# Kernel tuning notes

Hardware: AMD Instinct MI355X
Metric: run time of the kernel (lower is better)

The kernel has to match this reference:

```python
import jax, jax.numpy as jnp
import numpy as np

N_NODES = 100000
N_EDGES = 1600000
D_IN = 128
D_OUT = 128


def setup_inputs() -> dict:
    key = jax.random.key(0)
    k1, k2, k3 = jax.random.split(key, 3)
    x = jax.random.normal(k1, (N_NODES, D_IN), dtype=jnp.float32)
    edge_index = jax.random.randint(k2, (2, N_EDGES), 0, N_NODES, dtype=jnp.int32)
    W = jax.random.normal(k3, (D_IN, D_OUT), dtype=jnp.float32) / np.sqrt(D_IN)
    b = jnp.zeros((D_OUT,), dtype=jnp.float32)
    return {"x": x, "edge_index": edge_index, "W": W, "b": b}


def reference(x, edge_index, W, b):
    """GCNConv (add self-loops, symmetric norm) + ReLU.
    out = relu(D^-1/2 (A+I) D^-1/2 X W + b)
    """
    N = x.shape[0]
    src, dst = edge_index[0], edge_index[1]
    loop = jnp.arange(N, dtype=src.dtype)
    src = jnp.concatenate([src, loop])  # [E+N]
    dst = jnp.concatenate([dst, loop])  # [E+N]

    # degree of target nodes (includes self-loop, so deg >= 1)
    deg = jax.ops.segment_sum(jnp.ones(dst.shape, dtype=x.dtype), dst,
                              num_segments=N)
    deg_inv_sqrt = jax.lax.rsqrt(deg)
    norm = deg_inv_sqrt[src] * deg_inv_sqrt[dst]  # [E+N]

    h = x @ W  # [N, D_OUT] — transform before aggregation (PyG GCNConv)
    msg = h[src] * norm[:, None]  # gather + normalize
    out = jax.ops.segment_sum(msg, dst, num_segments=N)  # scatter-add
    return jax.nn.relu(out + b)
```

## Files before the change

### kernel.cpp

```cpp
#include <hip/hip_runtime.h>

#define N_NODES 100000
#define N_EDGES 1600000
#define D 128
#define SUBW 32
#define NSUB2 3125
#define NC 196
#define BSH 9
#define BMSK 511
#define CAPC 12288
#define CAP3 9728
#define CAPS2 1024
#define CHUNK3 4096
#define BIND_BLOCKS ((N_EDGES + CHUNK3 - 1) / CHUNK3)
#define GEMM_BLOCKS ((N_NODES + 63) / 64)
#define STAGE_MAX (CHUNK3 + NC * 16)
#define NGRP (STAGE_MAX / 16)
#define CCSTRIDE 16

typedef __attribute__((ext_vector_type(8))) short short8;
typedef __attribute__((ext_vector_type(4))) float float4v;

__device__ inline unsigned short f2bf(float f) {
    unsigned u = __float_as_uint(f);
    unsigned r = (u + 0x7fffu + ((u >> 16) & 1u)) >> 16;
    return (unsigned short)r;
}
__device__ inline float bflo(unsigned int p) { return __uint_as_float(p << 16); }
__device__ inline float bfhi(unsigned int p) { return __uint_as_float(p & 0xffff0000u); }

__global__ void probe_convert_kernel(const unsigned int* __restrict__ xw,
                                     const void* __restrict__ b,
                                     int* __restrict__ flag, float* __restrict__ bfv,
                                     int* __restrict__ ccnt) {
    __shared__ int cnt;
    if (threadIdx.x == 0) cnt = 0;
    __syncthreads();
    unsigned low = xw[threadIdx.x] & 0xFFFFu;
    unsigned e = (low >> 7) & 0xFFu;
    atomicAdd(&cnt, (int)((e == 0u) || (e >= 107u && e <= 147u)));
    __syncthreads();
    int m = (cnt >= 192);
    if (threadIdx.x == 0) *flag = m;
    if (threadIdx.x < D)
        bfv[threadIdx.x] = m ? bflo(((const unsigned short*)b)[threadIdx.x])
                             : ((const float*)b)[threadIdx.x];
    for (int i = threadIdx.x; i < NC * CCSTRIDE; i += 256) ccnt[i] = 0;
}

__global__ void __launch_bounds__(256) fused_bingemm_kernel(
        const int* __restrict__ src, const int* __restrict__ dst,
        int* __restrict__ ccnt, unsigned* __restrict__ recg,
        const void* __restrict__ xv, const void* __restrict__ Wv,
        const int* __restrict__ flag, unsigned short* __restrict__ h) {
    __shared__ union {
        struct {
            unsigned stg[STAGE_MAX];
            int cnt[NC], cpad[NC], ofs[NC], base[NC], place[NC];
            unsigned short g2b[NGRP];
            int tot;
        } b;
        unsigned short Wt[D * 136];
    } u;

    int tid = threadIdx.x;

    if (blockIdx.x < BIND_BLOCKS) {
        int e0 = blockIdx.x * CHUNK3;
        int e1 = e0 + CHUNK3 < N_EDGES ? e0 + CHUNK3 : N_EDGES;
        if (tid < NC) u.b.cnt[tid] = 0;
        __syncthreads();

        unsigned recs[16];
        int bks[16];
        #pragma unroll
        for (int k = 0; k < 4; ++k) {
            int i = e0 + tid * 4 + k * 1024;
            if (i + 3 < e1) {
                int4 d4 = *(const int4*)&dst[i];
                int4 s4 = *(const int4*)&src[i];
                recs[k * 4 + 0] = (unsigned)s4.x | ((unsigned)(d4.x & BMSK) << 17); bks[k * 4 + 0] = d4.x >> BSH;
                recs[k * 4 + 1] = (unsigned)s4.y | ((unsigned)(d4.y & BMSK) << 17); bks[k * 4 + 1] = d4.y >> BSH;
                recs[k * 4 + 2] = (unsigned)s4.z | ((unsigned)(d4.z & BMSK) << 17); bks[k * 4 + 2] = d4.z >> BSH;
                recs[k * 4 + 3] = (unsigned)s4.w | ((unsigned)(d4.w & BMSK) << 17); bks[k * 4 + 3] = d4.w >> BSH;
            } else {
                bks[k * 4 + 0] = -1; bks[k * 4 + 1] = -1; bks[k * 4 + 2] = -1; bks[k * 4 + 3] = -1;
                recs[k * 4 + 0] = 0; recs[k * 4 + 1] = 0; recs[k * 4 + 2] = 0; recs[k * 4 + 3] = 0;
            }
        }
        #pragma unroll
        for (int k = 0; k < 16; ++k)
            if (bks[k] >= 0) atomicAdd(&u.b.cnt[bks[k]], 1);
        __syncthreads();

        if (tid < NC) {
            int c = u.b.cnt[tid];
            int p = (c + 15) & ~15;
            u.b.cpad[tid] = p;
            u.b.base[tid] = p ? atomicAdd(&ccnt[tid * CCSTRIDE], p) : 0;
        }
        __syncthreads();
        if (tid == 0) {
            int s = 0;
            for (int k = 0; k < NC; ++k) { u.b.ofs[k] = s; u.b.place[k] = s; s += u.b.cpad[k]; }
            u.b.tot = s;
        }
        __syncthreads();
        if (tid < NC) {
            int o = u.b.ofs[tid], e = o + u.b.cpad[tid];
            for (int j = o + u.b.cnt[tid]; j < e; ++j) u.b.stg[j] = 0xFFFFFFFFu;
            for (int g = o >> 4; g < (e >> 4); ++g) u.b.g2b[g] = (unsigned short)tid;
        }
        __syncthreads();

        #pragma unroll
        for (int k = 0; k < 16; ++k)
            if (bks[k] >= 0) {
                int p = atomicAdd(&u.b.place[bks[k]], 1);
                u.b.stg[p] = recs[k];
            }
        __syncthreads();

        int tot_ = u.b.tot;
        for (int j = tid * 4; j < tot_; j += 1024) {
            int lo = u.b.g2b[j >> 4];
            int gi = u.b.base[lo] + (j - u.b.ofs[lo]);
            if (gi < CAPC)
                *(uint4*)&recg[(size_t)lo * CAPC + gi] = *(const uint4*)&u.b.stg[j];
        }
    } else {
        int bid2 = blockIdx.x - BIND_BLOCKS;
        int m = *flag;
        for (int idx = tid; idx < D * D; idx += 256) {
            int k = idx >> 7, c = idx & 127;
            u.Wt[c * 136 + k] = m ? ((const unsigned short*)Wv)[idx]
                                  : f2bf(((const float*)Wv)[idx]);
        }
        __syncthreads();

        int wave = tid >> 6, lane = tid & 63;
        int row0 = (bid2 * 4 + wave) * 16;
        if (row0 >= N_NODES) return;
        int r = lane & 15, quad = lane >> 4;

        short8 a[4];
        if (m) {
            const unsigned short* xr = (const unsigned short*)xv + (size_t)(row0 + r) * D + quad * 8;
            #pragma unroll
            for (int t = 0; t < 4; ++t) a[t] = *(const short8*)(xr + t * 32);
        } else {
            const float* xr = (const float*)xv + (size_t)(row0 + r) * D + quad * 8;
            #pragma unroll
            for (int t = 0; t < 4; ++t) {
                float4 f0 = *(const float4*)(xr + t * 32);
                float4 f1 = *(const float4*)(xr + t * 32 + 4);
                a[t][0] = (short)f2bf(f0.x); a[t][1] = (short)f2bf(f0.y);
                a[t][2] = (short)f2bf(f0.z); a[t][3] = (short)f2bf(f0.w);
                a[t][4] = (short)f2bf(f1.x); a[t][5] = (short)f2bf(f1.y);
                a[t][6] = (short)f2bf(f1.z); a[t][7] = (short)f2bf(f1.w);
            }
        }

        #pragma unroll
        for (int ct = 0; ct < 8; ++ct) {
            int col0 = ct * 16;
            float4v c = {0.f, 0.f, 0.f, 0.f};
            #pragma unroll
            for (int t = 0; t < 4; ++t) {
                short8 bfr = *(const short8*)&u.Wt[(col0 + r) * 136 + t * 32 + quad * 8];
                c = __builtin_amdgcn_mfma_f32_16x16x32_bf16(a[t], bfr, c, 0, 0, 0);
            }
            #pragma unroll
            for (int reg = 0; reg < 4; ++reg) {
                int orow = row0 + quad * 4 + reg;
                h[(size_t)orow * D + col0 + r] = f2bf(c[reg]);
            }
        }
    }
}

__global__ void __launch_bounds__(1024) sortdeg_kernel(
        unsigned* __restrict__ recg, const int* __restrict__ ccnt,
        int* __restrict__ deg, int* __restrict__ nodeofs, float* __restrict__ dis) {
    __shared__ int hist[512];
    __shared__ int ofs[512];
    __shared__ int place[512];
    __shared__ int wsum[8];
    __shared__ __align__(16) unsigned s_srt[CAP3];

    int b = blockIdx.x, tid = threadIdx.x;
    if (tid < 512) hist[tid] = 0;
    __syncthreads();
    int count = ccnt[b * CCSTRIDE]; if (count > CAPC) count = CAPC;
    const unsigned* r = recg + (size_t)b * CAPC;
    for (int i = tid * 4; i + 3 < count; i += 4096) {
        uint4 w4 = *(const uint4*)&r[i];
        if (w4.x != 0xFFFFFFFFu) atomicAdd(&hist[w4.x >> 17], 1);
        if (w4.y != 0xFFFFFFFFu) atomicAdd(&hist[w4.y >> 17], 1);
        if (w4.z != 0xFFFFFFFFu) atomicAdd(&hist[w4.z >> 17], 1);
        if (w4.w != 0xFFFFFFFFu) atomicAdd(&hist[w4.w >> 17], 1);
    }
    __syncthreads();

    int lane = tid & 63, wave = tid >> 6;
    int h0 = 0, v = 0;
    if (tid < 512) {
        h0 = hist[tid];
        v = h0;
        #pragma unroll
        for (int dsh = 1; dsh < 64; dsh <<= 1) {
            int uu = __shfl_up(v, dsh);
            if (lane >= dsh) v += uu;
        }
        if (lane == 63) wsum[wave] = v;
    }
    __syncthreads();
    if (tid < 512) {
        int wbase = 0;
        #pragma unroll
        for (int k = 0; k < 8; ++k) if (k < wave) wbase += wsum[k];
        int e0v = wbase + v - h0;
        ofs[tid] = e0v; place[tid] = e0v;
        int n = b * 512 + tid;
        deg[n] = h0;
        nodeofs[n] = e0v;
        dis[n] = rsqrtf((float)(h0 + 1));
    }
    __syncthreads();

    for (int i = tid * 4; i + 3 < count; i += 4096) {
        uint4 w4 = *(const uint4*)&r[i];
        if (w4.x != 0xFFFFFFFFu) { int p = atomicAdd(&place[w4.x >> 17], 1); if (p < CAP3) s_srt[p] = w4.x & 0x1FFFFu; }
        if (w4.y != 0xFFFFFFFFu) { int p = atomicAdd(&place[w4.y >> 17], 1); if (p < CAP3) s_srt[p] = w4.y & 0x1FFFFu; }
        if (w4.z != 0xFFFFFFFFu) { int p = atomicAdd(&place[w4.z >> 17], 1); if (p < CAP3) s_srt[p] = w4.z & 0x1FFFFu; }
        if (w4.w != 0xFFFFFFFFu) { int p = atomicAdd(&place[w4.w >> 17], 1); if (p < CAP3) s_srt[p] = w4.w & 0x1FFFFu; }
    }
    __syncthreads();

    int total = ofs[511] + hist[511];
    int totR = (total + 15) & ~15; if (totR > CAP3) totR = CAP3;
    unsigned* w = recg + (size_t)b * CAPC;
    for (int j = tid * 4; j < totR; j += 4096)
        *(uint4*)&w[j] = *(const uint4*)&s_srt[j];
}

__global__ void __launch_bounds__(256) agg5_kernel(
        const unsigned* __restrict__ srt2, const int* __restrict__ nodeofs,
        const int* __restrict__ deg, const float* __restrict__ dis,
        const float* __restrict__ bfv, const int* __restrict__ flag,
        const unsigned short* __restrict__ h, void* __restrict__ out) {
    __shared__ unsigned srt[CAPS2];
    __shared__ int l_ofs[SUBW];
    __shared__ int l_deg[SUBW];
    __shared__ float lbias[D];

    int sub = blockIdx.x, tid = threadIdx.x;
    int n0 = sub * SUBW;
    int B = n0 >> BSH, loc0 = n0 & BMSK;
    if (tid < SUBW) {
        l_ofs[tid] = nodeofs[B * 512 + loc0 + tid];
        l_deg[tid] = deg[n0 + tid];
    }
    if (tid < D) lbias[tid] = bfv[tid];
    __syncthreads();

    int base0 = l_ofs[0];
    int span = (l_ofs[SUBW - 1] + l_deg[SUBW - 1]) - base0;
    if (span > CAPS2) span = CAPS2;
    if (span > CAP3 - base0) span = CAP3 - base0;
    const unsigned* sb = srt2 + (size_t)B * CAPC + base0;
    for (int i = tid; i < span; i += 256) srt[i] = sb[i];
    __syncthreads();

    const uint4* h4 = (const uint4*)h;
    int wave = tid >> 6, lane = tid & 63;
    int q = lane >> 4, c16 = lane & 15;
    int m = *flag;

    for (int t = 0; t < 8; ++t) {
        int nl = wave * 8 + t;
        int n = n0 + nl;
        int o = l_ofs[nl] - base0;
        int cnt = l_deg[nl];
        int e_end = o + cnt; if (e_end > span) e_end = span;

        uint4 sp = make_uint4(0u, 0u, 0u, 0u);
        if (q == 0) sp = h4[(size_t)n * 16 + c16];

        float acc[8] = {0.f, 0.f, 0.f, 0.f, 0.f, 0.f, 0.f, 0.f};
        int j = o + q;
        for (; j + 4 < e_end; j += 8) {
            unsigned s0 = srt[j];
            unsigned s1 = srt[j + 4];
            uint4 p0 = h4[(size_t)s0 * 16 + c16];
            uint4 p1 = h4[(size_t)s1 * 16 + c16];
            float w0 = dis[s0], w1 = dis[s1];
            acc[0] += w0 * bflo(p0.x); acc[1] += w0 * bfhi(p0.x);
            acc[2] += w0 * bflo(p0.y); acc[3] += w0 * bfhi(p0.y);
            acc[4] += w0 * bflo(p0.z); acc[5] += w0 * bfhi(p0.z);
            acc[6] += w0 * bflo(p0.w); acc[7] += w0 * bfhi(p0.w);
            acc[0] += w1 * bflo(p1.x); acc[1] += w1 * bfhi(p1.x);
            acc[2] += w1 * bflo(p1.y); acc[3] += w1 * bfhi(p1.y);
            acc[4] += w1 * bflo(p1.z); acc[5] += w1 * bfhi(p1.z);
            acc[6] += w1 * bflo(p1.w); acc[7] += w1 * bfhi(p1.w);
        }
        if (j < e_end) {
            unsigned s0 = srt[j];
            uint4 p0 = h4[(size_t)s0 * 16 + c16];
            float w0 = dis[s0];
            acc[0] += w0 * bflo(p0.x); acc[1] += w0 * bfhi(p0.x);
            acc[2] += w0 * bflo(p0.y); acc[3] += w0 * bfhi(p0.y);
            acc[4] += w0 * bflo(p0.z); acc[5] += w0 * bfhi(p0.z);
            acc[6] += w0 * bflo(p0.w); acc[7] += w0 * bfhi(p0.w);
        }
        #pragma unroll
        for (int i = 0; i < 8; ++i) {
            acc[i] += __shfl_xor(acc[i], 16);
            acc[i] += __shfl_xor(acc[i], 32);
        }

        if (q == 0) {
            float dn = rsqrtf((float)(cnt + 1));
            float v[8];
            v[0] = fmaxf(dn * (acc[0] + dn * bflo(sp.x)) + lbias[c16 * 8 + 0], 0.f);
            v[1] = fmaxf(dn * (acc[1] + dn * bfhi(sp.x)) + lbias[c16 * 8 + 1], 0.f);
            v[2] = fmaxf(dn * (acc[2] + dn * bflo(sp.y)) + lbias[c16 * 8 + 2], 0.f);
            v[3] = fmaxf(dn * (acc[3] + dn * bfhi(sp.y)) + lbias[c16 * 8 + 3], 0.f);
            v[4] = fmaxf(dn * (acc[4] + dn * bflo(sp.z)) + lbias[c16 * 8 + 4], 0.f);
            v[5] = fmaxf(dn * (acc[5] + dn * bfhi(sp.z)) + lbias[c16 * 8 + 5], 0.f);
            v[6] = fmaxf(dn * (acc[6] + dn * bflo(sp.w)) + lbias[c16 * 8 + 6], 0.f);
            v[7] = fmaxf(dn * (acc[7] + dn * bfhi(sp.w)) + lbias[c16 * 8 + 7], 0.f);
            if (m) {
                uint4 pk;
                pk.x = ((unsigned)f2bf(v[1]) << 16) | f2bf(v[0]);
                pk.y = ((unsigned)f2bf(v[3]) << 16) | f2bf(v[2]);
                pk.z = ((unsigned)f2bf(v[5]) << 16) | f2bf(v[4]);
                pk.w = ((unsigned)f2bf(v[7]) << 16) | f2bf(v[6]);
                ((uint4*)out)[(size_t)n * 16 + c16] = pk;
            } else {
                float4 f0 = make_float4(v[0], v[1], v[2], v[3]);
                float4 f1 = make_float4(v[4], v[5], v[6], v[7]);
                float4* of = (float4*)((float*)out + (size_t)n * D + c16 * 8);
                of[0] = f0; of[1] = f1;
            }
        }
    }
}

extern "C" void kernel_launch(void* const* d_in, const int* in_sizes, int n_in,
                              void* d_out, int out_size, void* d_ws, size_t ws_size,
                              hipStream_t stream) {
    const void* x = nullptr; const int* ei = nullptr;
    const void* W = nullptr; const void* b = nullptr;
    for (int i = 0; i < n_in; ++i) {
        if      (in_sizes[i] == N_NODES * D) x  = d_in[i];
        else if (in_sizes[i] == 2 * N_EDGES) ei = (const int*)d_in[i];
        else if (in_sizes[i] == D * D)       W  = d_in[i];
        else if (in_sizes[i] == D)           b  = d_in[i];
    }
    if (!x || !ei || !W || !b) {
        x = d_in[0]; ei = (const int*)d_in[1]; W = d_in[2]; b = d_in[3];
    }
    const int* src = ei;
    const int* dst = ei + N_EDGES;

    char* ws = (char*)d_ws;
    int*      flag    = (int*)ws;
    int*      ccnt    = (int*)(ws + 16);
    float*    bfv     = (float*)(ccnt + NC * CCSTRIDE);
    int*      deg     = (int*)(bfv + D);
    int*      nodeofs = deg + NC * 512;
    float*    dis     = (float*)(nodeofs + NC * 512);
    unsigned* recg    = (unsigned*)(dis + NC * 512);
    unsigned short* h = (unsigned short*)(recg + (size_t)NC * CAPC);

    probe_convert_kernel<<<1, 256, 0, stream>>>((const unsigned int*)x, b, flag, bfv, ccnt);

    fused_bingemm_kernel<<<BIND_BLOCKS + GEMM_BLOCKS, 256, 0, stream>>>(
        src, dst, ccnt, recg, x, W, flag, h);

    sortdeg_kernel<<<NC, 1024, 0, stream>>>(recg, ccnt, deg, nodeofs, dis);

    agg5_kernel<<<NSUB2, 256, 0, stream>>>(recg, nodeofs, deg, dis, bfv, flag, h, d_out);
}
```

Measured before the change: 244.1 us.

## Refuse GEMM with per-bucket sort instead of binning; preconvert W once

```diff
diff --git a/kernel.cpp b/kernel.cpp
--- a/kernel.cpp
+++ b/kernel.cpp
@@ -13,7 +13,7 @@
 #define CAPS2 1024
 #define CHUNK3 4096
 #define BIND_BLOCKS ((N_EDGES + CHUNK3 - 1) / CHUNK3)
-#define GEMM_BLOCKS ((N_NODES + 63) / 64)
+#define GEMM2_BLOCKS ((N_NODES + 127) / 128)
 #define STAGE_MAX (CHUNK3 + NC * 16)
 #define NGRP (STAGE_MAX / 16)
 #define CCSTRIDE 16
@@ -31,7 +31,9 @@
 
 __global__ void probe_convert_kernel(const unsigned int* __restrict__ xw,
                                      const void* __restrict__ b,
+                                     const void* __restrict__ Wv,
                                      int* __restrict__ flag, float* __restrict__ bfv,
+                                     unsigned short* __restrict__ Wbf,
                                      int* __restrict__ ccnt) {
     __shared__ int cnt;
     if (threadIdx.x == 0) cnt = 0;
@@ -45,101 +47,160 @@
     if (threadIdx.x < D)
         bfv[threadIdx.x] = m ? bflo(((const unsigned short*)b)[threadIdx.x])
                              : ((const float*)b)[threadIdx.x];
+    for (int i = threadIdx.x; i < D * D; i += 256)
+        Wbf[i] = m ? ((const unsigned short*)Wv)[i] : f2bf(((const float*)Wv)[i]);
     for (int i = threadIdx.x; i < NC * CCSTRIDE; i += 256) ccnt[i] = 0;
 }
 
-__global__ void __launch_bounds__(256) fused_bingemm_kernel(
+__global__ void __launch_bounds__(256) binD_kernel(
         const int* __restrict__ src, const int* __restrict__ dst,
-        int* __restrict__ ccnt, unsigned* __restrict__ recg,
-        const void* __restrict__ xv, const void* __restrict__ Wv,
+        int* __restrict__ ccnt, unsigned* __restrict__ recg) {
+    __shared__ __align__(16) unsigned stg[STAGE_MAX];
+    __shared__ int cnt[NC], cpad[NC], ofs[NC], base[NC], place[NC];
+    __shared__ unsigned short g2b[NGRP];
+    __shared__ int tot;
+
+    int tid = threadIdx.x;
+    int e0 = blockIdx.x * CHUNK3;
+    int e1 = e0 + CHUNK3 < N_EDGES ? e0 + CHUNK3 : N_EDGES;
+    if (tid < NC) cnt[tid] = 0;
+    __syncthreads();
+
+    unsigned recs[16];
+    int bks[16];
+    #pragma unroll
+    for (int k = 0; k < 4; ++k) {
+        int i = e0 + tid * 4 + k * 1024;
+        if (i + 3 < e1) {
+            int4 d4 = *(const int4*)&dst[i];
+            int4 s4 = *(const int4*)&src[i];
+            recs[k * 4 + 0] = (unsigned)s4.x | ((unsigned)(d4.x & BMSK) << 17); bks[k * 4 + 0] = d4.x >> BSH;
+            recs[k * 4 + 1] = (unsigned)s4.y | ((unsigned)(d4.y & BMSK) << 17); bks[k * 4 + 1] = d4.y >> BSH;
+            recs[k * 4 + 2] = (unsigned)s4.z | ((unsigned)(d4.z & BMSK) << 17); bks[k * 4 + 2] = d4.z >> BSH;
+            recs[k * 4 + 3] = (unsigned)s4.w | ((unsigned)(d4.w & BMSK) << 17); bks[k * 4 + 3] = d4.w >> BSH;
+        } else {
+            bks[k * 4 + 0] = -1; bks[k * 4 + 1] = -1; bks[k * 4 + 2] = -1; bks[k * 4 + 3] = -1;
+            recs[k * 4 + 0] = 0; recs[k * 4 + 1] = 0; recs[k * 4 + 2] = 0; recs[k * 4 + 3] = 0;
+        }
+    }
+    #pragma unroll
+    for (int k = 0; k < 16; ++k)
+        if (bks[k] >= 0) atomicAdd(&cnt[bks[k]], 1);
+    __syncthreads();
+
+    if (tid < NC) {
+        int c = cnt[tid];
+        int p = (c + 15) & ~15;
+        cpad[tid] = p;
+        base[tid] = p ? atomicAdd(&ccnt[tid * CCSTRIDE], p) : 0;
+    }
+    __syncthreads();
+    if (tid == 0) {
+        int s = 0;
+        for (int k = 0; k < NC; ++k) { ofs[k] = s; place[k] = s; s += cpad[k]; }
+        tot = s;
+    }
+    __syncthreads();
+    if (tid < NC) {
+        int o = ofs[tid], e = o + cpad[tid];
+        for (int j = o + cnt[tid]; j < e; ++j) stg[j] = 0xFFFFFFFFu;
+        for (int g = o >> 4; g < (e >> 4); ++g) g2b[g] = (unsigned short)tid;
+    }
+    __syncthreads();
+
+    #pragma unroll
+    for (int k = 0; k < 16; ++k)
+        if (bks[k] >= 0) {
+            int p = atomicAdd(&place[bks[k]], 1);
+            stg[p] = recs[k];
+        }
+    __syncthreads();
+
+    int tot_ = tot;
+    for (int j = tid * 4; j < tot_; j += 1024) {
+        int lo = g2b[j >> 4];
+        int gi = base[lo] + (j - ofs[lo]);
+        if (gi < CAPC)
+            *(uint4*)&recg[(size_t)lo * CAPC + gi] = *(const uint4*)&stg[j];
+    }
+}
+
+__global__ void __launch_bounds__(512) fused_sortgemm_kernel(
+        unsigned* __restrict__ recg, const int* __restrict__ ccnt,
+        int* __restrict__ deg, int* __restrict__ nodeofs, float* __restrict__ dis,
+        const void* __restrict__ xv, const unsigned short* __restrict__ Wbf,
         const int* __restrict__ flag, unsigned short* __restrict__ h) {
     __shared__ union {
         struct {
-            unsigned stg[STAGE_MAX];
-            int cnt[NC], cpad[NC], ofs[NC], base[NC], place[NC];
-            unsigned short g2b[NGRP];
-            int tot;
-        } b;
+            int hist[512], ofs[512], place[512], wsum[8];
+            __align__(16) unsigned s_srt[CAP3];
+        } s;
         unsigned short Wt[D * 136];
     } u;
 
     int tid = threadIdx.x;
 
-    if (blockIdx.x < BIND_BLOCKS) {
-        int e0 = blockIdx.x * CHUNK3;
-        int e1 = e0 + CHUNK3 < N_EDGES ? e0 + CHUNK3 : N_EDGES;
-        if (tid < NC) u.b.cnt[tid] = 0;
-        __syncthreads();
-
-        unsigned recs[16];
-        int bks[16];
+    if (blockIdx.x < NC) {
+        int b = blockIdx.x;
+        u.s.hist[tid] = 0;
+        __syncthreads();
+        int count = ccnt[b * CCSTRIDE]; if (count > CAPC) count = CAPC;
+        const unsigned* r = recg + (size_t)b * CAPC;
+        for (int i = tid * 4; i + 3 < count; i += 2048) {
+            uint4 w4 = *(const uint4*)&r[i];
+            if (w4.x != 0xFFFFFFFFu) atomicAdd(&u.s.hist[w4.x >> 17], 1);
+            if (w4.y != 0xFFFFFFFFu) atomicAdd(&u.s.hist[w4.y >> 17], 1);
+            if (w4.z != 0xFFFFFFFFu) atomicAdd(&u.s.hist[w4.z >> 17], 1);
+            if (w4.w != 0xFFFFFFFFu) atomicAdd(&u.s.hist[w4.w >> 17], 1);
+        }
+        __syncthreads();
+
+        int lane = tid & 63, wave = tid >> 6;
+        int h0 = u.s.hist[tid];
+        int v = h0;
         #pragma unroll
-        for (int k = 0; k < 4; ++k) {
-            int i = e0 + tid * 4 + k * 1024;
-            if (i + 3 < e1) {
-                int4 d4 = *(const int4*)&dst[i];
-                int4 s4 = *(const int4*)&src[i];
-                recs[k * 4 + 0] = (unsigned)s4.x | ((unsigned)(d4.x & BMSK) << 17); bks[k * 4 + 0] = d4.x >> BSH;
-                recs[k * 4 + 1] = (unsigned)s4.y | ((unsigned)(d4.y & BMSK) << 17); bks[k * 4 + 1] = d4.y >> BSH;
-                recs[k * 4 + 2] = (unsigned)s4.z | ((unsigned)(d4.z & BMSK) << 17); bks[k * 4 + 2] = d4.z >> BSH;
-                recs[k * 4 + 3] = (unsigned)s4.w | ((unsigned)(d4.w & BMSK) << 17); bks[k * 4 + 3] = d4.w >> BSH;
-            } else {
-                bks[k * 4 + 0] = -1; bks[k * 4 + 1] = -1; bks[k * 4 + 2] = -1; bks[k * 4 + 3] = -1;
-                recs[k * 4 + 0] = 0; recs[k * 4 + 1] = 0; recs[k * 4 + 2] = 0; recs[k * 4 + 3] = 0;
-            }
-        }
+        for (int dsh = 1; dsh < 64; dsh <<= 1) {
+            int uu = __shfl_up(v, dsh);
+            if (lane >= dsh) v += uu;
+        }
+        if (lane == 63) u.s.wsum[wave] = v;
+        __syncthreads();
+        int wbase = 0;
         #pragma unroll
-        for (int k = 0; k < 16; ++k)
-            if (bks[k] >= 0) atomicAdd(&u.b.cnt[bks[k]], 1);
-        __syncthreads();
-
-        if (tid < NC) {
-            int c = u.b.cnt[tid];
-            int p = (c + 15) & ~15;
-            u.b.cpad[tid] = p;
-            u.b.base[tid] = p ? atomicAdd(&ccnt[tid * CCSTRIDE], p) : 0;
-        }
-        __syncthreads();
-        if (tid == 0) {
-            int s = 0;
-            for (int k = 0; k < NC; ++k) { u.b.ofs[k] = s; u.b.place[k] = s; s += u.b.cpad[k]; }
-            u.b.tot = s;
-        }
-        __syncthreads();
-        if (tid < NC) {
-            int o = u.b.ofs[tid], e = o + u.b.cpad[tid];
-            for (int j = o + u.b.cnt[tid]; j < e; ++j) u.b.stg[j] = 0xFFFFFFFFu;
-            for (int g = o >> 4; g < (e >> 4); ++g) u.b.g2b[g] = (unsigned short)tid;
-        }
-        __syncthreads();
-
-        #pragma unroll
-        for (int k = 0; k < 16; ++k)
-            if (bks[k] >= 0) {
-                int p = atomicAdd(&u.b.place[bks[k]], 1);
-                u.b.stg[p] = recs[k];
-            }
-        __syncthreads();
-
-        int tot_ = u.b.tot;
-        for (int j = tid * 4; j < tot_; j += 1024) {
-            int lo = u.b.g2b[j >> 4];
-            int gi = u.b.base[lo] + (j - u.b.ofs[lo]);
-            if (gi < CAPC)
-                *(uint4*)&recg[(size_t)lo * CAPC + gi] = *(const uint4*)&u.b.stg[j];
-        }
+        for (int k = 0; k < 8; ++k) if (k < wave) wbase += u.s.wsum[k];
+        int e0v = wbase + v - h0;
+        u.s.ofs[tid] = e0v; u.s.place[tid] = e0v;
+        int n = b * 512 + tid;
+        deg[n] = h0;
+        nodeofs[n] = e0v;
+        dis[n] = rsqrtf((float)(h0 + 1));
+        __syncthreads();
+
+        for (int i = tid * 4; i + 3 < count; i += 2048) {
+            uint4 w4 = *(const uint4*)&r[i];
+            if (w4.x != 0xFFFFFFFFu) { int p = atomicAdd(&u.s.place[w4.x >> 17], 1); if (p < CAP3) u.s.s_srt[p] = w4.x & 0x1FFFFu; }
+            if (w4.y != 0xFFFFFFFFu) { int p = atomicAdd(&u.s.place[w4.y >> 17], 1); if (p < CAP3) u.s.s_srt[p] = w4.y & 0x1FFFFu; }
+            if (w4.z != 0xFFFFFFFFu) { int p = atomicAdd(&u.s.place[w4.z >> 17], 1); if (p < CAP3) u.s.s_srt[p] = w4.z & 0x1FFFFu; }
+            if (w4.w != 0xFFFFFFFFu) { int p = atomicAdd(&u.s.place[w4.w >> 17], 1); if (p < CAP3) u.s.s_srt[p] = w4.w & 0x1FFFFu; }
+        }
+        __syncthreads();
+
+        int total = u.s.ofs[511] + u.s.hist[511];
+        int totR = (total + 15) & ~15; if (totR > CAP3) totR = CAP3;
+        unsigned* w = recg + (size_t)b * CAPC;
+        for (int j = tid * 4; j < totR; j += 2048)
+            *(uint4*)&w[j] = *(const uint4*)&u.s.s_srt[j];
     } else {
-        int bid2 = blockIdx.x - BIND_BLOCKS;
+        int bid2 = blockIdx.x - NC;
         int m = *flag;
-        for (int idx = tid; idx < D * D; idx += 256) {
+        for (int idx = tid; idx < D * D; idx += 512) {
             int k = idx >> 7, c = idx & 127;
-            u.Wt[c * 136 + k] = m ? ((const unsigned short*)Wv)[idx]
-                                  : f2bf(((const float*)Wv)[idx]);
+            u.Wt[c * 136 + k] = Wbf[idx];
         }
         __syncthreads();
 
         int wave = tid >> 6, lane = tid & 63;
-        int row0 = (bid2 * 4 + wave) * 16;
+        int row0 = (bid2 * 8 + wave) * 16;
         if (row0 >= N_NODES) return;
         int r = lane & 15, quad = lane >> 4;
 
@@ -177,71 +238,6 @@
             }
         }
     }
-}
-
-__global__ void __launch_bounds__(1024) sortdeg_kernel(
-        unsigned* __restrict__ recg, const int* __restrict__ ccnt,
-        int* __restrict__ deg, int* __restrict__ nodeofs, float* __restrict__ dis) {
-    __shared__ int hist[512];
-    __shared__ int ofs[512];
-    __shared__ int place[512];
-    __shared__ int wsum[8];
-    __shared__ __align__(16) unsigned s_srt[CAP3];
-
-    int b = blockIdx.x, tid = threadIdx.x;
-    if (tid < 512) hist[tid] = 0;
-    __syncthreads();
-    int count = ccnt[b * CCSTRIDE]; if (count > CAPC) count = CAPC;
-    const unsigned* r = recg + (size_t)b * CAPC;
-    for (int i = tid * 4; i + 3 < count; i += 4096) {
-        uint4 w4 = *(const uint4*)&r[i];
-        if (w4.x != 0xFFFFFFFFu) atomicAdd(&hist[w4.x >> 17], 1);
-        if (w4.y != 0xFFFFFFFFu) atomicAdd(&hist[w4.y >> 17], 1);
-        if (w4.z != 0xFFFFFFFFu) atomicAdd(&hist[w4.z >> 17], 1);
-        if (w4.w != 0xFFFFFFFFu) atomicAdd(&hist[w4.w >> 17], 1);
-    }
-    __syncthreads();
-
-    int lane = tid & 63, wave = tid >> 6;
-    int h0 = 0, v = 0;
-    if (tid < 512) {
-        h0 = hist[tid];
-        v = h0;
-        #pragma unroll
-        for (int dsh = 1; dsh < 64; dsh <<= 1) {
-            int uu = __shfl_up(v, dsh);
-            if (lane >= dsh) v += uu;
-        }
-        if (lane == 63) wsum[wave] = v;
-    }
-    __syncthreads();
-    if (tid < 512) {
-        int wbase = 0;
-        #pragma unroll
-        for (int k = 0; k < 8; ++k) if (k < wave) wbase += wsum[k];
-        int e0v = wbase + v - h0;
-        ofs[tid] = e0v; place[tid] = e0v;
-        int n = b * 512 + tid;
-        deg[n] = h0;
-        nodeofs[n] = e0v;
-        dis[n] = rsqrtf((float)(h0 + 1));
-    }
-    __syncthreads();
-
-    for (int i = tid * 4; i + 3 < count; i += 4096) {
-        uint4 w4 = *(const uint4*)&r[i];
-        if (w4.x != 0xFFFFFFFFu) { int p = atomicAdd(&place[w4.x >> 17], 1); if (p < CAP3) s_srt[p] = w4.x & 0x1FFFFu; }
-        if (w4.y != 0xFFFFFFFFu) { int p = atomicAdd(&place[w4.y >> 17], 1); if (p < CAP3) s_srt[p] = w4.y & 0x1FFFFu; }
-        if (w4.z != 0xFFFFFFFFu) { int p = atomicAdd(&place[w4.z >> 17], 1); if (p < CAP3) s_srt[p] = w4.z & 0x1FFFFu; }
-        if (w4.w != 0xFFFFFFFFu) { int p = atomicAdd(&place[w4.w >> 17], 1); if (p < CAP3) s_srt[p] = w4.w & 0x1FFFFu; }
-    }
-    __syncthreads();
-
-    int total = ofs[511] + hist[511];
-    int totR = (total + 15) & ~15; if (totR > CAP3) totR = CAP3;
-    unsigned* w = recg + (size_t)b * CAPC;
-    for (int j = tid * 4; j < totR; j += 4096)
-        *(uint4*)&w[j] = *(const uint4*)&s_srt[j];
 }
 
 __global__ void __launch_bounds__(256) agg5_kernel(
@@ -368,18 +364,20 @@
     int*      flag    = (int*)ws;
     int*      ccnt    = (int*)(ws + 16);
     float*    bfv     = (float*)(ccnt + NC * CCSTRIDE);
-    int*      deg     = (int*)(bfv + D);
+    unsigned short* Wbf = (unsigned short*)(bfv + D);
+    int*      deg     = (int*)(Wbf + D * D);
     int*      nodeofs = deg + NC * 512;
     float*    dis     = (float*)(nodeofs + NC * 512);
     unsigned* recg    = (unsigned*)(dis + NC * 512);
     unsigned short* h = (unsigned short*)(recg + (size_t)NC * CAPC);
 
-    probe_convert_kernel<<<1, 256, 0, stream>>>((const unsigned int*)x, b, flag, bfv, ccnt);
-
-    fused_bingemm_kernel<<<BIND_BLOCKS + GEMM_BLOCKS, 256, 0, stream>>>(
-        src, dst, ccnt, recg, x, W, flag, h);
-
-    sortdeg_kernel<<<NC, 1024, 0, stream>>>(recg, ccnt, deg, nodeofs, dis);
+    probe_convert_kernel<<<1, 256, 0, stream>>>((const unsigned int*)x, b, W,
+                                                flag, bfv, Wbf, ccnt);
+
+    binD_kernel<<<BIND_BLOCKS, 256, 0, stream>>>(src, dst, ccnt, recg);
+
+    fused_sortgemm_kernel<<<NC + GEMM2_BLOCKS, 512, 0, stream>>>(
+        recg, ccnt, deg, nodeofs, dis, x, Wbf, flag, h);
 
     agg5_kernel<<<NSUB2, 256, 0, stream>>>(recg, nodeofs, deg, dis, bfv, flag, h, d_out);
 }
```

New measurement: 242.9 us. About the same (-0.5%).
